# Kernel tuning notes

Measured on AMD Instinct MI355X. Metric: run time of the kernel, lower is better.

## Reference

```python
import jax, jax.numpy as jnp
import numpy as np

MT = 0.1
MF = 0.1

def _damp_mask(F_dims, T_dims, dtype):
    # Faithful to original: BOTH terms are functions of t (term2 uses t, not f).
    t = jnp.arange(T_dims, dtype=dtype)
    term1 = 1.0 - MT * jnp.abs(t - T_dims / 2) / (T_dims / 2)
    term2 = 1.0 - MF * jnp.abs(t - F_dims / 2) / (F_dims / 2)
    c_t = term1 * term2                      # [T]
    return jnp.broadcast_to(c_t, (F_dims, T_dims))  # [F, T], constant over f


def setup_inputs() -> dict:
    key = jax.random.key(0)
    k1, k2 = jax.random.split(key)
    x = jax.random.normal(k1, (32, 64, 128, 256), dtype=jnp.float32)
    W = jax.random.normal(k2, (128, 64, 3, 3), dtype=jnp.float32) * 0.05
    b = jnp.zeros((128,), dtype=jnp.float32)
    return {"x": x, "W": W, "b": b}


def reference(x, W, b):
    # x: [N, C, F, T]
    F_dims, T_dims = x.shape[2], x.shape[3]
    C = _damp_mask(F_dims, T_dims, x.dtype)          # [F, T]
    xd = x * C[None, None, :, :]
    y = jax.lax.conv_general_dilated(
        xd, W,
        window_strides=(1, 1),
        padding=((1, 1), (1, 1)),
        dimension_numbers=("NCHW", "OIHW", "NCHW"),
    )
    return y + b[None, :, None, None]
```

## Files before the change

### kernel.cpp

```cpp
#include <hip/hip_runtime.h>

typedef __attribute__((ext_vector_type(8))) short bf16x8;
typedef __attribute__((ext_vector_type(16))) float f32x16;

#define CPs  72
#define ROWS 130
#define SLOT (ROWS * CPs)
#define FPB  8

__device__ __forceinline__ unsigned short f2bf(float v) {
    unsigned u = __builtin_bit_cast(unsigned, v);
    return (unsigned short)((u + 0x7fffu + ((u >> 16) & 1u)) >> 16);
}

__device__ __forceinline__ float dampf(float tt) {
    return (1.0f - 0.1f * fabsf(tt - 128.f) * (1.f / 128.f))
         * (1.0f - 0.1f * fabsf(tt - 64.f) * (1.f / 64.f));
}

__global__ __launch_bounds__(256) void prep_w(const float* __restrict__ W,
                                              unsigned short* __restrict__ Wr) {
    int id = blockIdx.x * 256 + threadIdx.x;
    if (id >= 9 * 128 * 64) return;
    int c = id & 63, o = (id >> 6) & 127, k9 = id >> 13;
    Wr[id] = f2bf(W[(o * 64 + c) * 9 + k9]);
}

__global__ __launch_bounds__(256) void damp_conv_mfma(
    const float* __restrict__ x, const unsigned short* __restrict__ Wr,
    const float* __restrict__ b, float* __restrict__ out)
{
    __shared__ unsigned short xs[3 * SLOT];

    const int tid  = threadIdx.x;
    const int lane = tid & 63;
    const int wid  = tid >> 6;
    const int q    = lane & 3;
    const int p16  = lane >> 2;
    const int lo32 = lane & 31;
    const int kg   = lane >> 5;

    const int raw = blockIdx.x;
    const int logical = (raw & 7) * 128 + (raw >> 3);
    const int n  = logical >> 5;
    const int th = (logical >> 4) & 1;
    const int f0 = (logical & 15) * FPB;

    const int tb = th * 128;
    const int oh = wid & 1;
    const int tw = wid >> 1;

    const unsigned selv = (q & 1) ? 0x07060302u : 0x05040100u;

    float dmp[2][4];
    #pragma unroll
    for (int s = 0; s < 2; ++s)
        #pragma unroll
        for (int j = 0; j < 4; ++j)
            dmp[s][j] = dampf((float)(tb + 64 * s + 4 * p16 + j));

    const int hside = (tid >> 6) & 1;
    const int hc    = tid & 63;
    const int t_h   = tb + (hside ? 128 : -1);
    const bool tok  = (unsigned)t_h < 256u;
    const float dmp_h = dampf((float)(tok ? t_h : 0));

    float4 rb[8];
    float  hv;

    auto issue_row = [&](int fg) {
        const bool fok = (unsigned)fg < 128u;
        #pragma unroll
        for (int j = 0; j < 8; ++j) {
            int c = wid * 16 + (j & 3) * 4 + q;
            const float* src = x + ((size_t)(n * 64 + c) * 128 + (fok ? fg : 0)) * 256
                             + tb + (j >> 2) * 64 + 4 * p16;
            rb[j] = fok ? *(const float4*)src : (float4){0.f, 0.f, 0.f, 0.f};
        }
        hv = 0.f;
        if (tid < 128 && fok && tok)
            hv = x[((size_t)(n * 64 + hc) * 128 + fg) * 256 + t_h];
    };

    auto write_row = [&](int slot) {
        unsigned short* dstb = &xs[slot * SLOT];
        #pragma unroll
        for (int j = 0; j < 8; ++j) {
            const int s  = j >> 2;
            const int c0 = wid * 16 + (j & 3) * 4;
            float4 v = rb[j];
            unsigned d0 = (unsigned)f2bf(v.x * dmp[s][0]) | ((unsigned)f2bf(v.y * dmp[s][1]) << 16);
            unsigned d1 = (unsigned)f2bf(v.z * dmp[s][2]) | ((unsigned)f2bf(v.w * dmp[s][3]) << 16);
            unsigned p0 = __shfl_xor((int)d0, 2);
            unsigned p1 = __shfl_xor((int)d1, 2);
            bool hi = (lane >> 1) & 1;
            unsigned own = hi ? d1 : d0;
            unsigned oth = hi ? p1 : p0;
            unsigned sown = __shfl_xor((int)own, 1);
            unsigned soth = __shfl_xor((int)oth, 1);
            bool b0 = q & 1, b1 = q & 2;
            unsigned a0 = b0 ? sown : own, a1 = b0 ? own : sown;
            unsigned g0 = b0 ? soth : oth, g1 = b0 ? oth : soth;
            unsigned e0 = b1 ? g0 : a0, e1 = b1 ? g1 : a1;
            unsigned e2 = b1 ? a0 : g0, e3 = b1 ? a1 : g1;
            unsigned r0 = __builtin_amdgcn_perm(e1, e0, selv);
            unsigned r1 = __builtin_amdgcn_perm(e3, e2, selv);
            unsigned* dst = (unsigned*)&dstb[(1 + 64 * s + lane) * CPs + c0];
            dst[0] = r0;
            dst[1] = r1;
        }
        if (tid < 128)
            dstb[(hside ? (ROWS - 1) : 0) * CPs + hc] = f2bf(hv * dmp_h);
    };

    f32x16 acc[2][2];

    auto mfma_kh = [&](int kh, int slot) {
        const unsigned short* sb = &xs[slot * SLOT];
        #pragma unroll
        for (int kw = 0; kw < 3; ++kw) {
            #pragma unroll
            for (int ks = 0; ks < 4; ++ks) {
                const int cb = ks * 16 + kg * 8;
                bf16x8 af[2];
                #pragma unroll
                for (int fm = 0; fm < 2; ++fm) {
                    int o = oh * 64 + fm * 32 + lo32;
                    af[fm] = *(const bf16x8*)(Wr + (((kh * 3 + kw) * 128 + o) << 6) + cb);
                }
                #pragma unroll
                for (int fn = 0; fn < 2; ++fn) {
                    int row = tw * 64 + fn * 32 + lo32 + kw;
                    bf16x8 bx = *(const bf16x8*)&sb[row * CPs + cb];
                    #pragma unroll
                    for (int fm = 0; fm < 2; ++fm)
                        acc[fm][fn] = __builtin_amdgcn_mfma_f32_32x32x16_bf16(
                            af[fm], bx, acc[fm][fn], 0, 0, 0);
                }
            }
        }
    };

    issue_row(f0 - 1); write_row(0);
    issue_row(f0);     write_row(1);
    issue_row(f0 + 1); write_row(2);
    __syncthreads();

    int sA = 0, sB = 1, sC = 2;

    #pragma unroll 1
    for (int i = 0; i < FPB; ++i) {
        const int f = f0 + i;
        if (i < FPB - 1) issue_row(f + 2);

        #pragma unroll
        for (int a = 0; a < 2; ++a)
            #pragma unroll
            for (int c2 = 0; c2 < 2; ++c2)
                #pragma unroll
                for (int e = 0; e < 16; ++e) acc[a][c2][e] = 0.f;

        mfma_kh(0, sA);
        mfma_kh(1, sB);
        mfma_kh(2, sC);

        #pragma unroll
        for (int fm = 0; fm < 2; ++fm) {
            #pragma unroll
            for (int fn = 0; fn < 2; ++fn) {
                int t = tb + tw * 64 + fn * 32 + lo32;
                #pragma unroll
                for (int reg = 0; reg < 16; ++reg) {
                    int o = oh * 64 + fm * 32 + (reg & 3) + 8 * (reg >> 2) + 4 * kg;
                    out[(((size_t)n * 128 + o) * 128 + f) * 256 + t] = acc[fm][fn][reg] + b[o];
                }
            }
        }

        __syncthreads();
        if (i < FPB - 1) write_row(sA);
        __syncthreads();
        int tmp = sA; sA = sB; sB = sC; sC = tmp;
    }
}

extern "C" void kernel_launch(void* const* d_in, const int* in_sizes, int n_in,
                              void* d_out, int out_size, void* d_ws, size_t ws_size,
                              hipStream_t stream) {
    const float* x = (const float*)d_in[0];
    const float* W = (const float*)d_in[1];
    const float* b = (const float*)d_in[2];
    float* out = (float*)d_out;
    unsigned short* Wr = (unsigned short*)d_ws;

    hipLaunchKernelGGL(prep_w, dim3(288), dim3(256), 0, stream, W, Wr);
    hipLaunchKernelGGL(damp_conv_mfma, dim3(1024), dim3(256), 0, stream, x, Wr, b, out);
}
```

Baseline: 281.1 us.

## Pre-pack damped bf16 channels-last padded input and stage it via direct LDS loads

A new prep kernel applies the damping mask to x, converts it to bf16 and writes a zero-padded channels-last buffer to workspace. The conv kernel then fills its LDS with global_load_lds into an XOR-swizzled layout instead of doing register shuffles and conversions inside the main loop. This is meant to take conversion and transpose work off the MFMA kernel's critical path and cut LDS bank conflicts. In exchange it adds a separate pass that writes and rereads about 140 MB of bf16 data, and the new path only runs when the workspace is large enough.

After: 326.2 us. 16.0% more time.

```diff
diff --git a/kernel.cpp b/kernel.cpp
--- a/kernel.cpp
+++ b/kernel.cpp
@@ -2,6 +2,14 @@
 
 typedef __attribute__((ext_vector_type(8))) short bf16x8;
 typedef __attribute__((ext_vector_type(16))) float f32x16;
+
+#define XD_F 130
+#define XD_T 258
+#define XD_C 64
+#define XD_ELEMS ((size_t)32 * XD_F * XD_T * XD_C)
+#define WS_NEEDED ((XD_ELEMS + (size_t)9 * 128 * 64) * 2)
+
+#define SLOTX (130 * 64)
 
 #define CPs  72
 #define ROWS 130
@@ -24,6 +32,201 @@
     if (id >= 9 * 128 * 64) return;
     int c = id & 63, o = (id >> 6) & 127, k9 = id >> 13;
     Wr[id] = f2bf(W[(o * 64 + c) * 9 + k9]);
+}
+
+__global__ __launch_bounds__(256) void prep_x(const float* __restrict__ x,
+                                              unsigned short* __restrict__ xd) {
+    __shared__ unsigned short tile[128 * 72];
+
+    const int tid  = threadIdx.x;
+    const int lane = tid & 63;
+    const int wid  = tid >> 6;
+    const int q    = lane & 3;
+    const int p16  = lane >> 2;
+    const int n = blockIdx.x >> 7, f = blockIdx.x & 127;
+
+    const unsigned selv = (q & 1) ? 0x07060302u : 0x05040100u;
+
+    float dmp[4][4];
+    #pragma unroll
+    for (int s = 0; s < 4; ++s)
+        #pragma unroll
+        for (int j = 0; j < 4; ++j)
+            dmp[s][j] = dampf((float)(64 * s + 4 * p16 + j));
+
+    const size_t gout = ((size_t)(n * XD_F + f + 1)) * XD_T * XD_C;
+
+    #pragma unroll 1
+    for (int half = 0; half < 2; ++half) {
+        const int tb2 = half * 128;
+        float4 rb[8];
+        #pragma unroll
+        for (int j = 0; j < 8; ++j) {
+            int c = wid * 16 + (j & 3) * 4 + q;
+            int s = j >> 2;
+            const float* src = x + ((size_t)(n * 64 + c) * 128 + f) * 256 + tb2 + s * 64 + 4 * p16;
+            rb[j] = *(const float4*)src;
+        }
+        if (half) __syncthreads();
+        #pragma unroll
+        for (int j = 0; j < 8; ++j) {
+            const int s  = j >> 2;
+            const int sg = half * 2 + s;
+            const int c0 = wid * 16 + (j & 3) * 4;
+            float4 v = rb[j];
+            unsigned d0 = (unsigned)f2bf(v.x * dmp[sg][0]) | ((unsigned)f2bf(v.y * dmp[sg][1]) << 16);
+            unsigned d1 = (unsigned)f2bf(v.z * dmp[sg][2]) | ((unsigned)f2bf(v.w * dmp[sg][3]) << 16);
+            unsigned p0 = __shfl_xor((int)d0, 2);
+            unsigned p1 = __shfl_xor((int)d1, 2);
+            bool hi = (lane >> 1) & 1;
+            unsigned own = hi ? d1 : d0;
+            unsigned oth = hi ? p1 : p0;
+            unsigned sown = __shfl_xor((int)own, 1);
+            unsigned soth = __shfl_xor((int)oth, 1);
+            bool b0 = q & 1, b1 = q & 2;
+            unsigned a0 = b0 ? sown : own, a1 = b0 ? own : sown;
+            unsigned g0 = b0 ? soth : oth, g1 = b0 ? oth : soth;
+            unsigned e0 = b1 ? g0 : a0, e1 = b1 ? g1 : a1;
+            unsigned e2 = b1 ? a0 : g0, e3 = b1 ? a1 : g1;
+            unsigned r0 = __builtin_amdgcn_perm(e1, e0, selv);
+            unsigned r1 = __builtin_amdgcn_perm(e3, e2, selv);
+            unsigned* dst = (unsigned*)&tile[(64 * s + lane) * 72 + c0];
+            dst[0] = r0;
+            dst[1] = r1;
+        }
+        __syncthreads();
+        #pragma unroll
+        for (int it = 0; it < 4; ++it) {
+            int g = it * 2048 + tid * 8;
+            int row = g >> 6, col = g & 63;
+            bf16x8 vv = *(const bf16x8*)&tile[row * 72 + col];
+            *(bf16x8*)&xd[gout + (size_t)(1 + tb2 + row) * 64 + col] = vv;
+        }
+    }
+    if (tid < 64) {
+        int r = tid >> 5, c2 = tid & 31;
+        unsigned* pz = (unsigned*)&xd[gout + (size_t)(r ? 257 : 0) * 64];
+        pz[c2] = 0u;
+    }
+    if (f == 0 || f == 127) {
+        size_t base = ((size_t)(n * XD_F + (f == 0 ? 0 : 129))) * XD_T * XD_C;
+        const bf16x8 z = {0, 0, 0, 0, 0, 0, 0, 0};
+        for (int i = tid; i < XD_T * XD_C / 8; i += 256)
+            *(bf16x8*)&xd[base + (size_t)i * 8] = z;
+    }
+}
+
+__global__ __launch_bounds__(256) void conv_dma(
+    const unsigned short* __restrict__ xd, const unsigned short* __restrict__ Wr,
+    const float* __restrict__ b, float* __restrict__ out)
+{
+    __shared__ unsigned short xs[3 * SLOTX];
+
+    const int tid  = threadIdx.x;
+    const int lane = tid & 63;
+    const int wid  = tid >> 6;
+    const int lo32 = lane & 31;
+    const int kg   = lane >> 5;
+
+    const int raw = blockIdx.x;
+    const int logical = (raw & 7) * 128 + (raw >> 3);
+    const int n  = logical >> 5;
+    const int th = (logical >> 4) & 1;
+    const int f0 = (logical & 15) * FPB;
+
+    const int tb = th * 128;
+    const int oh = wid & 1;
+    const int tw = wid >> 1;
+
+    auto stage_dma = [&](int fg, int slot) {
+        const unsigned short* gbase = xd + ((size_t)(n * XD_F + fg + 1) * XD_T + tb) * 64;
+        #pragma unroll
+        for (int w = 0; w < 4; ++w) {
+            int ch = w * 256 + tid;
+            int r = ch >> 3, p = ch & 7;
+            int ps = p ^ (r & 7);
+            const unsigned short* src = gbase + r * 64 + ps * 8;
+            __builtin_amdgcn_global_load_lds(
+                (const __attribute__((address_space(1))) void*)src,
+                (__attribute__((address_space(3))) void*)&xs[slot * SLOTX + w * 2048 + wid * 512],
+                16, 0, 0);
+        }
+        if (tid < 16) {
+            int r = 128 + (tid >> 3), p = tid & 7;
+            int ps = p ^ (r & 7);
+            bf16x8 v = *(const bf16x8*)(gbase + r * 64 + ps * 8);
+            *(bf16x8*)&xs[slot * SLOTX + r * 64 + p * 8] = v;
+        }
+    };
+
+    f32x16 acc[2][2];
+
+    auto mfma_kh = [&](int kh, int slot) {
+        const unsigned short* sb = &xs[slot * SLOTX];
+        #pragma unroll
+        for (int kw = 0; kw < 3; ++kw) {
+            #pragma unroll
+            for (int ks = 0; ks < 4; ++ks) {
+                bf16x8 af[2];
+                #pragma unroll
+                for (int fm = 0; fm < 2; ++fm) {
+                    int o = oh * 64 + fm * 32 + lo32;
+                    af[fm] = *(const bf16x8*)(Wr + (((kh * 3 + kw) * 128 + o) << 6) + ks * 16 + kg * 8);
+                }
+                #pragma unroll
+                for (int fn = 0; fn < 2; ++fn) {
+                    int row = tw * 64 + fn * 32 + lo32 + kw;
+                    int p = (ks * 2 + kg) ^ (row & 7);
+                    bf16x8 bx = *(const bf16x8*)&sb[row * 64 + p * 8];
+                    #pragma unroll
+                    for (int fm = 0; fm < 2; ++fm)
+                        acc[fm][fn] = __builtin_amdgcn_mfma_f32_32x32x16_bf16(
+                            af[fm], bx, acc[fm][fn], 0, 0, 0);
+                }
+            }
+        }
+    };
+
+    stage_dma(f0 - 1, 0);
+    stage_dma(f0,     1);
+    stage_dma(f0 + 1, 2);
+    __syncthreads();
+
+    int sA = 0, sB = 1, sC = 2;
+
+    #pragma unroll 1
+    for (int i = 0; i < FPB; ++i) {
+        const int f = f0 + i;
+
+        #pragma unroll
+        for (int a = 0; a < 2; ++a)
+            #pragma unroll
+            for (int c2 = 0; c2 < 2; ++c2)
+                #pragma unroll
+                for (int e = 0; e < 16; ++e) acc[a][c2][e] = 0.f;
+
+        mfma_kh(0, sA);
+        mfma_kh(1, sB);
+        mfma_kh(2, sC);
+
+        #pragma unroll
+        for (int fm = 0; fm < 2; ++fm) {
+            #pragma unroll
+            for (int fn = 0; fn < 2; ++fn) {
+                int t = tb + tw * 64 + fn * 32 + lo32;
+                #pragma unroll
+                for (int reg = 0; reg < 16; ++reg) {
+                    int o = oh * 64 + fm * 32 + (reg & 3) + 8 * (reg >> 2) + 4 * kg;
+                    out[(((size_t)n * 128 + o) * 128 + f) * 256 + t] = acc[fm][fn][reg] + b[o];
+                }
+            }
+        }
+
+        __syncthreads();
+        if (i < FPB - 1) stage_dma(f + 2, sA);
+        __syncthreads();
+        int tmp = sA; sA = sB; sB = sC; sC = tmp;
+    }
 }
 
 __global__ __launch_bounds__(256) void damp_conv_mfma(
@@ -191,8 +394,16 @@
     const float* W = (const float*)d_in[1];
     const float* b = (const float*)d_in[2];
     float* out = (float*)d_out;
-    unsigned short* Wr = (unsigned short*)d_ws;
-
-    hipLaunchKernelGGL(prep_w, dim3(288), dim3(256), 0, stream, W, Wr);
-    hipLaunchKernelGGL(damp_conv_mfma, dim3(1024), dim3(256), 0, stream, x, Wr, b, out);
-}
+
+    if (ws_size >= WS_NEEDED) {
+        unsigned short* xd = (unsigned short*)d_ws;
+        unsigned short* Wr = xd + XD_ELEMS;
+        hipLaunchKernelGGL(prep_w, dim3(288), dim3(256), 0, stream, W, Wr);
+        hipLaunchKernelGGL(prep_x, dim3(4096), dim3(256), 0, stream, x, xd);
+        hipLaunchKernelGGL(conv_dma, dim3(1024), dim3(256), 0, stream, xd, Wr, b, out);
+    } else {
+        unsigned short* Wr = (unsigned short*)d_ws;
+        hipLaunchKernelGGL(prep_w, dim3(288), dim3(256), 0, stream, W, Wr);
+        hipLaunchKernelGGL(damp_conv_mfma, dim3(1024), dim3(256), 0, stream, x, Wr, b, out);
+    }
+}
```
